# Kernel tuning notes

Measured on AMD Instinct MI355X. Metric: run time of the kernel, lower is better.

Reference implementation:

```python
import jax, jax.numpy as jnp
import numpy as np

NUM_LAYERS = 3


def setup_inputs() -> dict:
    key = jax.random.key(0)
    k1, k2, k3 = jax.random.split(key, 3)
    B, LT, LC, F = 16, 256, 768, 256
    batch_target = jax.random.normal(k1, (B, LT, F), dtype=jnp.float32)
    batch_claim = jax.random.normal(k2, (B, LC, F), dtype=jnp.float32)
    # adjacency is accepted but mathematically unused (original masked_fill is non-in-place and discarded)
    batch_adj = jax.random.randint(jax.random.fold_in(key, 7), (B, LT + LC, LT + LC), 0, 2, dtype=jnp.int32)
    # per-layer trans_linear weights, nn.Linear(F, F, bias=False): y = x @ W.T, W is [out, in]
    W_trans = jax.random.normal(k3, (NUM_LAYERS, F, F), dtype=jnp.float32) * (1.0 / np.sqrt(F))
    return {"batch_target": batch_target, "batch_claim": batch_claim, "batch_adj": batch_adj, "W_trans": W_trans}


def _gcn_layer(node_rep, W):
    # dot attention: score[b,i,j] = <h_i, h_j>  (symmetric all-pairs dot product)
    # NOTE: original's masked_fill(batch_adj == 0, -1e9) is NOT in-place and its
    # result is discarded, so no masking is applied -- reproduced faithfully here.
    corr = jnp.einsum('bif,bjf->bij', node_rep, node_rep)
    attn = jax.nn.softmax(corr, axis=2)              # softmax over j (dim=2)
    trans = jnp.einsum('blf,gf->blg', node_rep, W)   # trans_linear (bias=False)
    node_out = jax.nn.relu(node_rep + jnp.einsum('bij,bjf->bif', attn, trans))
    return node_out, attn


def reference(batch_target, batch_claim, batch_adj, W_trans):
    target_len = batch_target.shape[1]
    node_rep = jnp.concatenate([batch_target, batch_claim], axis=1)  # [B, L, F]
    all_node_rep, all_corr_score = (), ()
    for i in range(NUM_LAYERS):
        node_rep, corr_score = _gcn_layer(node_rep, W_trans[i])
        all_node_rep = all_node_rep + (node_rep,)
        all_corr_score = all_corr_score + (corr_score,)
        # gcn_dropout: identity in eval mode
    target_rep = node_rep[:, :target_len, :]
    claim_rep = node_rep[:, target_len:, :]
    return (target_rep, claim_rep, all_node_rep, all_corr_score)
```

## Files before the change

### kernel.cpp

```cpp
#include <hip/hip_runtime.h>

typedef _Float16 h16;
typedef _Float16 h16x8 __attribute__((ext_vector_type(8)));
typedef _Float16 h16x4 __attribute__((ext_vector_type(4)));
typedef float    f32x4 __attribute__((ext_vector_type(4)));

#define NBATCH 16
#define LROWS  1024
#define FDIM   256

#define OFF_TGT 0ull
#define OFF_CLM 1048576ull
#define OFF_NR  4194304ull
#define OFF_AT  16777216ull

__device__ __forceinline__ void split2(float x, h16& h, h16& l) {
    h = (h16)x;
    l = (h16)(x - (float)h);
}

typedef const __attribute__((address_space(1))) void gvoid;
typedef __attribute__((address_space(3))) void lvoid;
__device__ __forceinline__ void gl_lds16(const void* g, void* l) {
    __builtin_amdgcn_global_load_lds((gvoid*)g, (lvoid*)l, 16, 0, 0);
}

__device__ const unsigned char TRI_I[36] = {
    0,0,0,0,0,0,0,0, 1,1,1,1,1,1,1, 2,2,2,2,2,2, 3,3,3,3,3, 4,4,4,4, 5,5,5, 6,6, 7};
__device__ const unsigned char TRI_J[36] = {
    0,1,2,3,4,5,6,7, 1,2,3,4,5,6,7, 2,3,4,5,6,7, 3,4,5,6,7, 4,5,6,7, 5,6,7, 6,7, 7};

__global__ __launch_bounds__(256) void convert_all(const float* __restrict__ tgt,
                                                   const float* __restrict__ clm,
                                                   const float* __restrict__ W,
                                                   h16* __restrict__ xh, h16* __restrict__ xl,
                                                   h16* __restrict__ wh) {
    int bid = blockIdx.x;
    if (bid < 4096) {
        size_t e = ((size_t)bid * 256 + threadIdx.x) * 4;
        int b  = (int)(e >> 18);
        int rf = (int)(e & 262143);
        int r  = rf >> 8, f = rf & 255;
        const float* src = (r < 256)
            ? tgt + ((size_t)b << 16) + ((size_t)r << 8) + f
            : clm + (size_t)b * 196608 + ((size_t)(r - 256) << 8) + f;
        f32x4 v = *(const f32x4*)src;
        h16x4 hv, lv;
#pragma unroll
        for (int j = 0; j < 4; ++j) { h16 hh, ll; split2(v[j], hh, ll); hv[j] = hh; lv[j] = ll; }
        *(h16x4*)(xh + e) = hv;
        *(h16x4*)(xl + e) = lv;
    } else {
        size_t e = ((size_t)(bid - 4096) * 256 + threadIdx.x) * 4;
        f32x4 v = *(const f32x4*)(W + e);
        h16x4 hv;
#pragma unroll
        for (int j = 0; j < 4; ++j) hv[j] = (h16)v[j];
        *(h16x4*)(wh + e) = hv;
    }
}

__global__ __launch_bounds__(256, 3) void gemm_ct(
    const h16* __restrict__ Xh, const h16* __restrict__ Xl,
    const h16* __restrict__ Wh,
    float* __restrict__ At, float2* __restrict__ part,
    h16* __restrict__ Th) {
    const int b = blockIdx.x & 15;
    const int u = blockIdx.x >> 4;
    const bool isCorr = u < 36;
    int it, jt;
    if (isCorr) { it = TRI_I[u]; jt = TRI_J[u]; }
    else        { int v = u - 36; it = v >> 1; jt = v & 1; }
    const int i0 = it * 128;
    const int j0 = jt * 128;
    const int t  = threadIdx.x;
    const int lane = t & 63, wid = t >> 6;
    const int wr = wid >> 1, wc = wid & 1;

    __shared__ alignas(16) char lds[32768];

    const size_t arow = ((size_t)b * LROWS + i0) * 256;
    const h16* bHp; const h16* bLp; size_t brow;
    if (isCorr) { bHp = Xh; bLp = Xl; brow = ((size_t)b * LROWS + j0) * 256; }
    else        { bHp = Wh; bLp = Xl; brow = (size_t)j0 * 256; }

    f32x4 acc[4][4];
#pragma unroll
    for (int i = 0; i < 4; ++i)
#pragma unroll
        for (int j = 0; j < 4; ++j) acc[i][j] = (f32x4){0.f, 0.f, 0.f, 0.f};

    const int grow = t >> 2;
    const int gq   = t & 3;

    for (int kt = 0; kt < 8; ++kt) {
        __syncthreads();
#pragma unroll
        for (int p = 0; p < 2; ++p) {
            int r = p * 64 + grow;
            size_t so = (size_t)r * 256 + kt * 32 + ((gq ^ ((r >> 1) & 3)) << 3);
            char* d = lds + p * 4096 + wid * 1024;
            gl_lds16(Xh + arow + so, d);
            gl_lds16(Xl + arow + so, d + 8192);
            gl_lds16(bHp + brow + so, d + 16384);
            if (isCorr) gl_lds16(bLp + brow + so, d + 24576);
        }
        __syncthreads();

        const int kq = lane >> 4;
        const int rA = wr * 64 + (lane & 15);
        const int rB = wc * 64 + (lane & 15);
        h16x8 ah[4], al[4], bh[4], bl[4];
#pragma unroll
        for (int mi = 0; mi < 4; ++mi) {
            int r   = rA + mi * 16;
            int off = r * 64 + ((kq ^ ((r >> 1) & 3)) << 4);
            ah[mi] = *(const h16x8*)(lds + off);
            al[mi] = *(const h16x8*)(lds + 8192 + off);
        }
#pragma unroll
        for (int nj = 0; nj < 4; ++nj) {
            int r   = rB + nj * 16;
            int off = r * 64 + ((kq ^ ((r >> 1) & 3)) << 4);
            bh[nj] = *(const h16x8*)(lds + 16384 + off);
            if (isCorr) bl[nj] = *(const h16x8*)(lds + 24576 + off);
        }
        __builtin_amdgcn_s_setprio(1);
#pragma unroll
        for (int mi = 0; mi < 4; ++mi)
#pragma unroll
            for (int nj = 0; nj < 4; ++nj) {
                acc[mi][nj] = __builtin_amdgcn_mfma_f32_16x16x32_f16(ah[mi], bh[nj], acc[mi][nj], 0, 0, 0);
                acc[mi][nj] = __builtin_amdgcn_mfma_f32_16x16x32_f16(al[mi], bh[nj], acc[mi][nj], 0, 0, 0);
                if (isCorr)
                    acc[mi][nj] = __builtin_amdgcn_mfma_f32_16x16x32_f16(ah[mi], bl[nj], acc[mi][nj], 0, 0, 0);
            }
        __builtin_amdgcn_s_setprio(0);
    }

    const int mBase = i0 + wr * 64;
    const int nBase = j0 + wc * 64;
    if (isCorr) {
        float* Cb = At + (size_t)b * LROWS * 1024;
#pragma unroll
        for (int mi = 0; mi < 4; ++mi)
#pragma unroll
            for (int nj = 0; nj < 4; ++nj) {
                int n  = nBase + nj * 16 + (lane & 15);
                int m0 = mBase + mi * 16 + ((lane >> 4) * 4);
#pragma unroll
                for (int rg = 0; rg < 4; ++rg)
                    Cb[(size_t)(m0 + rg) * 1024 + n] = acc[mi][nj][rg];
            }
        {
            const int chunk = jt * 2 + wc;
#pragma unroll
            for (int mi = 0; mi < 4; ++mi)
#pragma unroll
                for (int rg = 0; rg < 4; ++rg) {
                    float v0 = acc[mi][0][rg], v1 = acc[mi][1][rg];
                    float v2 = acc[mi][2][rg], v3 = acc[mi][3][rg];
                    float mx = fmaxf(fmaxf(v0, v1), fmaxf(v2, v3));
#pragma unroll
                    for (int off = 8; off >= 1; off >>= 1) mx = fmaxf(mx, __shfl_xor(mx, off, 64));
                    float s = __expf(v0 - mx) + __expf(v1 - mx) + __expf(v2 - mx) + __expf(v3 - mx);
#pragma unroll
                    for (int off = 8; off >= 1; off >>= 1) s += __shfl_xor(s, off, 64);
                    if ((lane & 15) == 0) {
                        int row = mBase + mi * 16 + ((lane >> 4) * 4) + rg;
                        part[((size_t)b * 1024 + row) * 16 + chunk] = make_float2(mx, s);
                    }
                }
        }
        if (it != jt) {
#pragma unroll
            for (int mi = 0; mi < 4; ++mi)
#pragma unroll
                for (int nj = 0; nj < 4; ++nj) {
                    int n  = nBase + nj * 16 + (lane & 15);
                    int m0 = mBase + mi * 16 + ((lane >> 4) * 4);
                    f32x4 vv = acc[mi][nj];
                    *(f32x4*)(Cb + (size_t)n * 1024 + m0) = vv;
                }
            const int chunk = it * 2 + wr;
#pragma unroll
            for (int nj = 0; nj < 4; ++nj) {
                float mx = -3.0e38f;
#pragma unroll
                for (int mi = 0; mi < 4; ++mi)
#pragma unroll
                    for (int rg = 0; rg < 4; ++rg) mx = fmaxf(mx, acc[mi][nj][rg]);
                mx = fmaxf(mx, __shfl_xor(mx, 16, 64));
                mx = fmaxf(mx, __shfl_xor(mx, 32, 64));
                float s = 0.f;
#pragma unroll
                for (int mi = 0; mi < 4; ++mi)
#pragma unroll
                    for (int rg = 0; rg < 4; ++rg) s += __expf(acc[mi][nj][rg] - mx);
                s += __shfl_xor(s, 16, 64);
                s += __shfl_xor(s, 32, 64);
                if (lane < 16) {
                    int n = nBase + nj * 16 + lane;
                    part[((size_t)b * 1024 + n) * 16 + chunk] = make_float2(mx, s);
                }
            }
        }
    } else {
#pragma unroll
        for (int mi = 0; mi < 4; ++mi)
#pragma unroll
            for (int nj = 0; nj < 4; ++nj) {
                int n  = nBase + nj * 16 + (lane & 15);
                int m0 = mBase + mi * 16 + ((lane >> 4) * 4);
                h16x4 hv;
#pragma unroll
                for (int rg = 0; rg < 4; ++rg) hv[rg] = (h16)acc[mi][nj][rg];
                size_t off = ((size_t)b * 256 + n) * 1024 + m0;
                *(h16x4*)(Th + off) = hv;
            }
    }
}

__global__ __launch_bounds__(256, 4) void gemm_pv(
    float* __restrict__ At,
    const h16* __restrict__ Th,
    const float2* __restrict__ part,
    h16* __restrict__ Xh, h16* __restrict__ Xl,
    float* __restrict__ NodeOut, float* __restrict__ OutBase, int last) {
    const int id   = blockIdx.x;
    const int xcd  = id & 7, rest = id >> 3;
    const int b    = (xcd << 1) | (rest & 1);
    const int mt   = rest >> 1;
    const int i0   = mt * 16;
    const int t    = threadIdx.x;
    const int lane = t & 63, wid = t >> 6;
    const int wc   = wid;

    __shared__ alignas(16) char lds[34816];
    __shared__ float2 sst[16];

    if (t < 16) {
        const float2* pp = part + ((size_t)b * 1024 + i0 + t) * 16;
        float2 v[16];
        float M = -3.0e38f;
#pragma unroll
        for (int c = 0; c < 16; ++c) { v[c] = pp[c]; M = fmaxf(M, v[c].x); }
        float S = 0.f;
#pragma unroll
        for (int c = 0; c < 16; ++c) S += v[c].y * __expf(v[c].x - M);
        sst[t] = make_float2(M, 1.0f / S);
    }
    __syncthreads();

    float* Arow = At + ((size_t)b * LROWS + i0) * 1024;
    const size_t tbase = (size_t)b * 256 * 1024;

    const int ar0 = t >> 4;
    const int aq  = t & 15;
    float2 st0 = sst[ar0];

    f32x4 acc[4];
#pragma unroll
    for (int i = 0; i < 4; ++i) acc[i] = (f32x4){0.f, 0.f, 0.f, 0.f};

    const int bgrow = t >> 3;
    const int bq    = t & 7;

    for (int kt = 0; kt < 16; ++kt) {
        f32x4 va0 = *(const f32x4*)(Arow + (size_t)ar0 * 1024 + kt * 64 + aq * 4);
        __syncthreads();

#pragma unroll
        for (int itr = 0; itr < 8; ++itr) {
            int g = itr * 32 + bgrow;
            size_t so = tbase + (size_t)g * 1024 + kt * 64 + ((bq ^ (g & 7)) << 3);
            char* d = lds + 2048 + itr * 4096 + wid * 1024;
            gl_lds16(Th + so, d);
        }

        f32x4 p0;
#pragma unroll
        for (int e = 0; e < 4; ++e) p0[e] = __expf(va0[e] - st0.x) * st0.y;
        *(f32x4*)(Arow + (size_t)ar0 * 1024 + kt * 64 + aq * 4) = p0;
        h16x4 h0;
#pragma unroll
        for (int e = 0; e < 4; ++e) h0[e] = (h16)p0[e];
        {
            int c = aq >> 1, hb = (aq & 1) * 8;
            int o0 = ar0 * 128 + ((c ^ (ar0 & 7)) * 16) + hb;
            *(h16x4*)(lds + o0) = h0;
        }
        __syncthreads();

        const int kq = lane >> 4;
        const int rA = lane & 15;
        __builtin_amdgcn_s_setprio(1);
#pragma unroll
        for (int s = 0; s < 2; ++s) {
            int ca = ((s * 4 + kq) ^ (rA & 7)) * 16;
            h16x8 ah = *(const h16x8*)(lds + rA * 128 + ca);
#pragma unroll
            for (int nf = 0; nf < 4; ++nf) {
                int g  = wc * 64 + nf * 16 + (lane & 15);
                int cb = ((s * 4 + kq) ^ (g & 7)) * 16;
                h16x8 bh = *(const h16x8*)(lds + 2048 + g * 128 + cb);
                acc[nf] = __builtin_amdgcn_mfma_f32_16x16x32_f16(ah, bh, acc[nf], 0, 0, 0);
            }
        }
        __builtin_amdgcn_s_setprio(0);
    }

#pragma unroll
    for (int nf = 0; nf < 4; ++nf) {
        int n = wc * 64 + nf * 16 + (lane & 15);
#pragma unroll
        for (int rg = 0; rg < 4; ++rg) {
            int m = i0 + ((lane >> 4) * 4) + rg;
            size_t off = ((size_t)b * LROWS + m) * FDIM + n;
            float res = (float)Xh[off] + (float)Xl[off];
            float y   = res + acc[nf][rg];
            y = y > 0.f ? y : 0.f;
            NodeOut[off] = y;
            h16 hh, ll; split2(y, hh, ll);
            Xh[off] = hh; Xl[off] = ll;
            if (last) {
                float* dst = (m < 256)
                    ? OutBase + OFF_TGT + ((size_t)b << 16) + ((size_t)m << 8) + n
                    : OutBase + OFF_CLM + (size_t)b * 196608 + ((size_t)(m - 256) << 8) + n;
                *dst = y;
            }
        }
    }
}

extern "C" void kernel_launch(void* const* d_in, const int* in_sizes, int n_in,
                              void* d_out, int out_size, void* d_ws, size_t ws_size,
                              hipStream_t stream) {
    (void)in_sizes; (void)n_in; (void)out_size; (void)ws_size;
    const float* tgt = (const float*)d_in[0];
    const float* clm = (const float*)d_in[1];
    const float* W   = (const float*)d_in[3];
    float* out = (float*)d_out;
    char*  ws  = (char*)d_ws;

    h16* xh = (h16*)(ws);
    h16* xl = (h16*)(ws + (8ull << 20));
    h16* th = (h16*)(ws + (16ull << 20));
    h16* wh = (h16*)(ws + (24ull << 20));
    float2* part = (float2*)(ws + (25ull << 20));

    convert_all<<<4288, 256, 0, stream>>>(tgt, clm, W, xh, xl, wh);

    for (int L = 0; L < 3; ++L) {
        float* at = out + OFF_AT + (size_t)L * 16777216ull;
        float* nr = out + OFF_NR + (size_t)L * 4194304ull;
        gemm_ct<<<832, 256, 0, stream>>>(xh, xl, wh + (size_t)L * 65536, at, part, th);
        gemm_pv<<<1024, 256, 0, stream>>>(at, th, part, xh, xl, nr, out, L == 2);
    }
}
```

Measured before the change: 254.7 us.

## Store fp16 chunk-local exponentials instead of fp32 scores; double PV row tile

```diff
diff --git a/kernel.cpp b/kernel.cpp
--- a/kernel.cpp
+++ b/kernel.cpp
@@ -63,7 +63,7 @@
 __global__ __launch_bounds__(256, 3) void gemm_ct(
     const h16* __restrict__ Xh, const h16* __restrict__ Xl,
     const h16* __restrict__ Wh,
-    float* __restrict__ At, float2* __restrict__ part,
+    h16* __restrict__ Ptil, float2* __restrict__ part,
     h16* __restrict__ Th) {
     const int b = blockIdx.x & 15;
     const int u = blockIdx.x >> 4;
@@ -141,17 +141,7 @@
     const int mBase = i0 + wr * 64;
     const int nBase = j0 + wc * 64;
     if (isCorr) {
-        float* Cb = At + (size_t)b * LROWS * 1024;
-#pragma unroll
-        for (int mi = 0; mi < 4; ++mi)
-#pragma unroll
-            for (int nj = 0; nj < 4; ++nj) {
-                int n  = nBase + nj * 16 + (lane & 15);
-                int m0 = mBase + mi * 16 + ((lane >> 4) * 4);
-#pragma unroll
-                for (int rg = 0; rg < 4; ++rg)
-                    Cb[(size_t)(m0 + rg) * 1024 + n] = acc[mi][nj][rg];
-            }
+        h16* Pb = Ptil + (size_t)b * LROWS * 1024;
         {
             const int chunk = jt * 2 + wc;
 #pragma unroll
@@ -163,25 +153,22 @@
                     float mx = fmaxf(fmaxf(v0, v1), fmaxf(v2, v3));
 #pragma unroll
                     for (int off = 8; off >= 1; off >>= 1) mx = fmaxf(mx, __shfl_xor(mx, off, 64));
-                    float s = __expf(v0 - mx) + __expf(v1 - mx) + __expf(v2 - mx) + __expf(v3 - mx);
+                    float e0 = __expf(v0 - mx), e1 = __expf(v1 - mx);
+                    float e2 = __expf(v2 - mx), e3 = __expf(v3 - mx);
+                    float s = e0 + e1 + e2 + e3;
 #pragma unroll
                     for (int off = 8; off >= 1; off >>= 1) s += __shfl_xor(s, off, 64);
-                    if ((lane & 15) == 0) {
-                        int row = mBase + mi * 16 + ((lane >> 4) * 4) + rg;
+                    int row = mBase + mi * 16 + ((lane >> 4) * 4) + rg;
+                    if ((lane & 15) == 0)
                         part[((size_t)b * 1024 + row) * 16 + chunk] = make_float2(mx, s);
-                    }
+                    size_t rb = (size_t)row * 1024 + nBase + (lane & 15);
+                    Pb[rb]      = (h16)e0;
+                    Pb[rb + 16] = (h16)e1;
+                    Pb[rb + 32] = (h16)e2;
+                    Pb[rb + 48] = (h16)e3;
                 }
         }
         if (it != jt) {
-#pragma unroll
-            for (int mi = 0; mi < 4; ++mi)
-#pragma unroll
-                for (int nj = 0; nj < 4; ++nj) {
-                    int n  = nBase + nj * 16 + (lane & 15);
-                    int m0 = mBase + mi * 16 + ((lane >> 4) * 4);
-                    f32x4 vv = acc[mi][nj];
-                    *(f32x4*)(Cb + (size_t)n * 1024 + m0) = vv;
-                }
             const int chunk = it * 2 + wr;
 #pragma unroll
             for (int nj = 0; nj < 4; ++nj) {
@@ -193,16 +180,24 @@
                 mx = fmaxf(mx, __shfl_xor(mx, 16, 64));
                 mx = fmaxf(mx, __shfl_xor(mx, 32, 64));
                 float s = 0.f;
+                h16x4 pt[4];
 #pragma unroll
                 for (int mi = 0; mi < 4; ++mi)
 #pragma unroll
-                    for (int rg = 0; rg < 4; ++rg) s += __expf(acc[mi][nj][rg] - mx);
+                    for (int rg = 0; rg < 4; ++rg) {
+                        float e = __expf(acc[mi][nj][rg] - mx);
+                        s += e;
+                        pt[mi][rg] = (h16)e;
+                    }
                 s += __shfl_xor(s, 16, 64);
                 s += __shfl_xor(s, 32, 64);
-                if (lane < 16) {
-                    int n = nBase + nj * 16 + lane;
+                int n = nBase + nj * 16 + (lane & 15);
+                if (lane < 16)
                     part[((size_t)b * 1024 + n) * 16 + chunk] = make_float2(mx, s);
-                }
+                size_t nb = (size_t)n * 1024 + mBase + ((lane >> 4) * 4);
+#pragma unroll
+                for (int mi = 0; mi < 4; ++mi)
+                    *(h16x4*)(Pb + nb + mi * 16) = pt[mi];
             }
         }
     } else {
@@ -222,24 +217,24 @@
 }
 
 __global__ __launch_bounds__(256, 4) void gemm_pv(
+    const h16* __restrict__ Ptil, const float2* __restrict__ part,
     float* __restrict__ At,
     const h16* __restrict__ Th,
-    const float2* __restrict__ part,
     h16* __restrict__ Xh, h16* __restrict__ Xl,
     float* __restrict__ NodeOut, float* __restrict__ OutBase, int last) {
     const int id   = blockIdx.x;
     const int xcd  = id & 7, rest = id >> 3;
     const int b    = (xcd << 1) | (rest & 1);
     const int mt   = rest >> 1;
-    const int i0   = mt * 16;
+    const int i0   = mt * 32;
     const int t    = threadIdx.x;
     const int lane = t & 63, wid = t >> 6;
     const int wc   = wid;
 
-    __shared__ alignas(16) char lds[34816];
-    __shared__ float2 sst[16];
-
-    if (t < 16) {
+    __shared__ alignas(16) char lds[38912];
+    float* sc = (float*)(lds + 36864);
+
+    if (t < 32) {
         const float2* pp = part + ((size_t)b * 1024 + i0 + t) * 16;
         float2 v[16];
         float M = -3.0e38f;
@@ -248,89 +243,98 @@
         float S = 0.f;
 #pragma unroll
         for (int c = 0; c < 16; ++c) S += v[c].y * __expf(v[c].x - M);
-        sst[t] = make_float2(M, 1.0f / S);
+        float inv = 1.0f / S;
+#pragma unroll
+        for (int c = 0; c < 16; ++c) sc[t * 16 + c] = __expf(v[c].x - M) * inv;
     }
     __syncthreads();
 
+    const h16* Prow = Ptil + ((size_t)b * LROWS + i0) * 1024;
     float* Arow = At + ((size_t)b * LROWS + i0) * 1024;
     const size_t tbase = (size_t)b * 256 * 1024;
 
-    const int ar0 = t >> 4;
-    const int aq  = t & 15;
-    float2 st0 = sst[ar0];
-
-    f32x4 acc[4];
-#pragma unroll
-    for (int i = 0; i < 4; ++i) acc[i] = (f32x4){0.f, 0.f, 0.f, 0.f};
-
-    const int bgrow = t >> 3;
-    const int bq    = t & 7;
+    const int ar = t >> 3;
+    const int ac = t & 7;
+
+    f32x4 acc[2][4];
+#pragma unroll
+    for (int i = 0; i < 2; ++i)
+#pragma unroll
+        for (int j = 0; j < 4; ++j) acc[i][j] = (f32x4){0.f, 0.f, 0.f, 0.f};
 
     for (int kt = 0; kt < 16; ++kt) {
-        f32x4 va0 = *(const f32x4*)(Arow + (size_t)ar0 * 1024 + kt * 64 + aq * 4);
+        h16x8 pt = *(const h16x8*)(Prow + (size_t)ar * 1024 + kt * 64 + ac * 8);
+        float s  = sc[ar * 16 + kt];
         __syncthreads();
 
 #pragma unroll
         for (int itr = 0; itr < 8; ++itr) {
-            int g = itr * 32 + bgrow;
-            size_t so = tbase + (size_t)g * 1024 + kt * 64 + ((bq ^ (g & 7)) << 3);
-            char* d = lds + 2048 + itr * 4096 + wid * 1024;
+            int g = itr * 32 + ar;
+            size_t so = tbase + (size_t)g * 1024 + kt * 64 + ((ac ^ (g & 7)) << 3);
+            char* d = lds + 4096 + itr * 4096 + wid * 1024;
             gl_lds16(Th + so, d);
         }
 
-        f32x4 p0;
-#pragma unroll
-        for (int e = 0; e < 4; ++e) p0[e] = __expf(va0[e] - st0.x) * st0.y;
-        *(f32x4*)(Arow + (size_t)ar0 * 1024 + kt * 64 + aq * 4) = p0;
-        h16x4 h0;
-#pragma unroll
-        for (int e = 0; e < 4; ++e) h0[e] = (h16)p0[e];
-        {
-            int c = aq >> 1, hb = (aq & 1) * 8;
-            int o0 = ar0 * 128 + ((c ^ (ar0 & 7)) * 16) + hb;
-            *(h16x4*)(lds + o0) = h0;
-        }
+        f32x4 plo, phi;
+#pragma unroll
+        for (int e = 0; e < 4; ++e) plo[e] = (float)pt[e] * s;
+#pragma unroll
+        for (int e = 0; e < 4; ++e) phi[e] = (float)pt[4 + e] * s;
+        *(f32x4*)(Arow + (size_t)ar * 1024 + kt * 64 + ac * 8)     = plo;
+        *(f32x4*)(Arow + (size_t)ar * 1024 + kt * 64 + ac * 8 + 4) = phi;
+        h16x8 a16;
+#pragma unroll
+        for (int e = 0; e < 4; ++e) { a16[e] = (h16)plo[e]; a16[4 + e] = (h16)phi[e]; }
+        *(h16x8*)(lds + ar * 128 + ((ac ^ (ar & 7)) << 4)) = a16;
         __syncthreads();
 
         const int kq = lane >> 4;
-        const int rA = lane & 15;
         __builtin_amdgcn_s_setprio(1);
 #pragma unroll
-        for (int s = 0; s < 2; ++s) {
-            int ca = ((s * 4 + kq) ^ (rA & 7)) * 16;
-            h16x8 ah = *(const h16x8*)(lds + rA * 128 + ca);
+        for (int s2 = 0; s2 < 2; ++s2) {
+            h16x8 ah[2], bh[4];
+#pragma unroll
+            for (int mi = 0; mi < 2; ++mi) {
+                int r = mi * 16 + (lane & 15);
+                ah[mi] = *(const h16x8*)(lds + r * 128 + (((s2 * 4 + kq) ^ (r & 7)) << 4));
+            }
 #pragma unroll
             for (int nf = 0; nf < 4; ++nf) {
-                int g  = wc * 64 + nf * 16 + (lane & 15);
-                int cb = ((s * 4 + kq) ^ (g & 7)) * 16;
-                h16x8 bh = *(const h16x8*)(lds + 2048 + g * 128 + cb);
-                acc[nf] = __builtin_amdgcn_mfma_f32_16x16x32_f16(ah, bh, acc[nf], 0, 0, 0);
-            }
+                int g = wc * 64 + nf * 16 + (lane & 15);
+                bh[nf] = *(const h16x8*)(lds + 4096 + g * 128 + (((s2 * 4 + kq) ^ (g & 7)) << 4));
+            }
+#pragma unroll
+            for (int mi = 0; mi < 2; ++mi)
+#pragma unroll
+                for (int nf = 0; nf < 4; ++nf)
+                    acc[mi][nf] = __builtin_amdgcn_mfma_f32_16x16x32_f16(ah[mi], bh[nf], acc[mi][nf], 0, 0, 0);
         }
         __builtin_amdgcn_s_setprio(0);
     }
 
 #pragma unroll
-    for (int nf = 0; nf < 4; ++nf) {
-        int n = wc * 64 + nf * 16 + (lane & 15);
-#pragma unroll
-        for (int rg = 0; rg < 4; ++rg) {
-            int m = i0 + ((lane >> 4) * 4) + rg;
-            size_t off = ((size_t)b * LROWS + m) * FDIM + n;
-            float res = (float)Xh[off] + (float)Xl[off];
-            float y   = res + acc[nf][rg];
-            y = y > 0.f ? y : 0.f;
-            NodeOut[off] = y;
-            h16 hh, ll; split2(y, hh, ll);
-            Xh[off] = hh; Xl[off] = ll;
-            if (last) {
-                float* dst = (m < 256)
-                    ? OutBase + OFF_TGT + ((size_t)b << 16) + ((size_t)m << 8) + n
-                    : OutBase + OFF_CLM + (size_t)b * 196608 + ((size_t)(m - 256) << 8) + n;
-                *dst = y;
-            }
-        }
-    }
+    for (int mi = 0; mi < 2; ++mi)
+#pragma unroll
+        for (int nf = 0; nf < 4; ++nf) {
+            int n = wc * 64 + nf * 16 + (lane & 15);
+#pragma unroll
+            for (int rg = 0; rg < 4; ++rg) {
+                int m = i0 + mi * 16 + ((lane >> 4) * 4) + rg;
+                size_t off = ((size_t)b * LROWS + m) * FDIM + n;
+                float res = (float)Xh[off] + (float)Xl[off];
+                float y   = res + acc[mi][nf][rg];
+                y = y > 0.f ? y : 0.f;
+                NodeOut[off] = y;
+                h16 hh, ll; split2(y, hh, ll);
+                Xh[off] = hh; Xl[off] = ll;
+                if (last) {
+                    float* dst = (m < 256)
+                        ? OutBase + OFF_TGT + ((size_t)b << 16) + ((size_t)m << 8) + n
+                        : OutBase + OFF_CLM + (size_t)b * 196608 + ((size_t)(m - 256) << 8) + n;
+                    *dst = y;
+                }
+            }
+        }
 }
 
 extern "C" void kernel_launch(void* const* d_in, const int* in_sizes, int n_in,
@@ -348,13 +352,14 @@
     h16* th = (h16*)(ws + (16ull << 20));
     h16* wh = (h16*)(ws + (24ull << 20));
     float2* part = (float2*)(ws + (25ull << 20));
+    h16* ptil = (h16*)(ws + (27ull << 20));
 
     convert_all<<<4288, 256, 0, stream>>>(tgt, clm, W, xh, xl, wh);
 
     for (int L = 0; L < 3; ++L) {
         float* at = out + OFF_AT + (size_t)L * 16777216ull;
         float* nr = out + OFF_NR + (size_t)L * 4194304ull;
-        gemm_ct<<<832, 256, 0, stream>>>(xh, xl, wh + (size_t)L * 65536, at, part, th);
-        gemm_pv<<<1024, 256, 0, stream>>>(at, th, part, xh, xl, nr, out, L == 2);
-    }
-}
+        gemm_ct<<<832, 256, 0, stream>>>(xh, xl, wh + (size_t)L * 65536, ptil, part, th);
+        gemm_pv<<<512, 256, 0, stream>>>(ptil, part, at, th, xh, xl, nr, out, L == 2);
+    }
+}
```

Result: faster. 227.4 us, median of 4 (-10.7%).
